# Kernel tuning notes

Hardware: AMD Instinct MI355X
Metric: run time of the kernel (lower is better)

The kernel has to match this reference:

```python
import jax, jax.numpy as jnp
import numpy as np

B, S, D = 2, 2048, 1024
H, DK = 16, 64
DFF = 4096
WINDOW = 128
GLOBAL = 16
EPS = 1e-5


def _layer_norm(x, g, b):
    mu = jnp.mean(x, axis=-1, keepdims=True)
    var = jnp.var(x, axis=-1, keepdims=True)
    return (x - mu) * jax.lax.rsqrt(var + EPS) * g + b


def setup_inputs() -> dict:
    key = jax.random.key(0)
    ks = jax.random.split(key, 12)
    s = 0.02
    inp = {
        "x": jax.random.normal(ks[0], (B, S, D), dtype=jnp.float32),
        "Wq": jax.random.normal(ks[1], (D, D), jnp.float32) * s,
        "bq": jnp.zeros((D,), jnp.float32),
        "Wk": jax.random.normal(ks[2], (D, D), jnp.float32) * s,
        "bk": jnp.zeros((D,), jnp.float32),
        "Wv": jax.random.normal(ks[3], (D, D), jnp.float32) * s,
        "bv": jnp.zeros((D,), jnp.float32),
        "Wo": jax.random.normal(ks[4], (D, D), jnp.float32) * s,
        "bo": jnp.zeros((D,), jnp.float32),
        "ln1_g": jnp.ones((D,), jnp.float32),
        "ln1_b": jnp.zeros((D,), jnp.float32),
        "W1": jax.random.normal(ks[5], (D, DFF), jnp.float32) * s,
        "b1": jnp.zeros((DFF,), jnp.float32),
        "W2": jax.random.normal(ks[6], (DFF, D), jnp.float32) * s,
        "b2": jnp.zeros((D,), jnp.float32),
        "ln2_g": jnp.ones((D,), jnp.float32),
        "ln2_b": jnp.zeros((D,), jnp.float32),
    }
    return inp


def _local_global_mask(seq_len):
    # token i attends to j iff |i-j| <= WINDOW, or i < GLOBAL, or j < GLOBAL
    i = jnp.arange(seq_len)[:, None]
    j = jnp.arange(seq_len)[None, :]
    m = jnp.abs(i - j) <= WINDOW
    m = m | (i < GLOBAL) | (j < GLOBAL)
    return m  # [S, S] bool


def reference(x, Wq, bq, Wk, bk, Wv, bv, Wo, bo, ln1_g, ln1_b,
              W1, b1, W2, b2, ln2_g, ln2_b):
    # --- self-attention sublayer (pre-norm residual) ---
    xn = _layer_norm(x, ln1_g, ln1_b)
    q = (xn @ Wq + bq).reshape(B, S, H, DK).transpose(0, 2, 1, 3)  # [B,H,S,DK]
    k = (xn @ Wk + bk).reshape(B, S, H, DK).transpose(0, 2, 1, 3)
    v = (xn @ Wv + bv).reshape(B, S, H, DK).transpose(0, 2, 1, 3)

    scores = jnp.einsum('bhqd,bhkd->bhqk', q, k) / jnp.sqrt(jnp.float32(DK))
    mask = _local_global_mask(S)  # [S,S]
    scores = jnp.where(mask[None, None], scores, jnp.float32(-jnp.inf))
    attn = jax.nn.softmax(scores, axis=-1)
    out = jnp.einsum('bhqk,bhkd->bhqd', attn, v)
    out = out.transpose(0, 2, 1, 3).reshape(B, S, D)
    out = out @ Wo + bo
    x = x + out

    # --- feed-forward sublayer (pre-norm residual) ---
    xn2 = _layer_norm(x, ln2_g, ln2_b)
    h = jax.nn.gelu(xn2 @ W1 + b1, approximate=False)
    ff = h @ W2 + b2
    x = x + ff
    return x
```

## Files before the change

kernel.cpp:

```cpp
#include <hip/hip_runtime.h>
#include <stdint.h>


typedef unsigned short u16;
typedef unsigned int   u32;
typedef __attribute__((ext_vector_type(8))) short  short8;
typedef __attribute__((ext_vector_type(4))) float  f32x4;

#define S_LEN   2048
#define D_MODEL 1024
#define ROWS    4096

__device__ __forceinline__ float bf2f(u16 u) {
  union { u32 i; float f; } v; v.i = ((u32)u) << 16; return v.f;
}
__device__ __forceinline__ float bflo(u32 u) {
  union { u32 i; float f; } v; v.i = u << 16; return v.f;
}
__device__ __forceinline__ float bfhi(u32 u) {
  union { u32 i; float f; } v; v.i = u & 0xffff0000u; return v.f;
}
__device__ __forceinline__ u16 f2bf(float f) {
  union { float f; u32 i; } v; v.f = f;
  u32 r = v.i + 0x7fffu + ((v.i >> 16) & 1u);
  return (u16)(r >> 16);
}

__device__ __forceinline__ void gld_lds16(const u16* g, u16* l) {
  __attribute__((address_space(3))) u32* lp =
      reinterpret_cast<__attribute__((address_space(3))) u32*>(
          reinterpret_cast<uintptr_t>(l));
  const __attribute__((address_space(1))) u32* gp =
      reinterpret_cast<const __attribute__((address_space(1))) u32*>(
          reinterpret_cast<uintptr_t>(g));
  __builtin_amdgcn_global_load_lds(gp, lp, 16, 0, 0);
}


#define GBAR  asm volatile("s_barrier" ::: "memory")
#define LGKM(n) asm volatile("s_waitcnt lgkmcnt(" #n ")" ::: "memory")
#define VM(n)   asm volatile("s_waitcnt vmcnt(" #n ")" ::: "memory")

#define STAGE_A(buf, t, hm) do {                                              \
    gld_lds16(pA##hm + (size_t)(t) * 64,      &Ald[buf][0][(hm)*4096 + ldst]);\
    gld_lds16(pA##hm + (size_t)(t) * 64 + 32, &Ald[buf][1][(hm)*4096 + ldst]);\
  } while (0)

#define STAGE_B(buf, t, hm) do {                                              \
    gld_lds16(pB##hm + (size_t)(t) * 64,      &Bld[buf][0][(hm)*4096 + ldst]);\
    gld_lds16(pB##hm + (size_t)(t) * 64 + 32, &Bld[buf][1][(hm)*4096 + ldst]);\
  } while (0)

#define READ_B(buf) do {                                                      \
    _Pragma("unroll") for (int nj = 0; nj < 4; ++nj) {                        \
      bfv[nj][0] = *(const short8*)&Bld[buf][0][brow + nj * 512];             \
      bfv[nj][1] = *(const short8*)&Bld[buf][1][brow + nj * 512]; }           \
  } while (0)

#define READ_A(buf, q) do {                                                   \
    af[(q)&1][0][0] = *(const short8*)&Ald[buf][0][arow + (2*(q)) * 512];     \
    af[(q)&1][0][1] = *(const short8*)&Ald[buf][1][arow + (2*(q)) * 512];     \
    af[(q)&1][1][0] = *(const short8*)&Ald[buf][0][arow + (2*(q)+1) * 512];   \
    af[(q)&1][1][1] = *(const short8*)&Ald[buf][1][arow + (2*(q)+1) * 512];   \
  } while (0)

#define MFMA_Q(q) do {                                                        \
    __builtin_amdgcn_s_setprio(1);                                            \
    _Pragma("unroll") for (int dm = 0; dm < 2; ++dm)                          \
    _Pragma("unroll") for (int kk = 0; kk < 2; ++kk)                          \
    _Pragma("unroll") for (int nj = 0; nj < 4; ++nj)                          \
      acc[2*(q)+dm][nj] = __builtin_amdgcn_mfma_f32_16x16x32_bf16(            \
          af[(q)&1][dm][kk], bfv[nj][kk], acc[2*(q)+dm][nj], 0, 0, 0);        \
    __builtin_amdgcn_s_setprio(0);                                            \
  } while (0)

template <int EPI, int KC, int LDK>
__global__ __launch_bounds__(512) void gemm256(
    const u16* __restrict__ A, const u16* __restrict__ Bt,
    const float* __restrict__ bias, u16* __restrict__ C0,
    u16* __restrict__ C1, int N)
{
  __shared__ __attribute__((aligned(16))) u16 Ald[2][2][256 * 32];
  __shared__ __attribute__((aligned(16))) u16 Bld[2][2][256 * 32];

  const int tid  = threadIdx.x;
  const int w    = tid >> 6;
  const int lane = tid & 63;
  const int wm   = w >> 2;
  const int wn   = w & 3;
  const int lm   = lane & 15;
  const int kq   = lane >> 4;
  const int bm   = blockIdx.y * 256;
  const int bn   = blockIdx.x * 256;
  const int kz   = blockIdx.z;

  const u16* Ak = A  + (size_t)kz * KC;
  const u16* Bk = Bt + (size_t)kz * KC;
  u16* C = kz ? C1 : C0;

  const int rslot = ((kq + (lm >> 1)) & 3) * 8;
  const int arow  = (wm * 128 + lm) * 32 + rslot;
  const int brow  = (wn * 64  + lm) * 32 + rslot;

  const int gcoff = (((lane & 3) - (lane >> 3)) & 3) * 8;
  const int srow  = w * 16 + (lane >> 2);
  const int ldst  = w * 512;

  const u16* pA0 = Ak + (size_t)(bm + srow) * LDK + gcoff;
  const u16* pA1 = pA0 + (size_t)128 * LDK;
  const u16* pB0 = Bk + (size_t)(bn + srow) * LDK + gcoff;
  const u16* pB1 = pB0 + (size_t)128 * LDK;

  f32x4 acc[8][4];
#pragma unroll
  for (int i = 0; i < 8; ++i)
#pragma unroll
    for (int j = 0; j < 4; ++j) acc[i][j] = (f32x4){0.f, 0.f, 0.f, 0.f};

  short8 af[2][2][2];
  short8 bfv[4][2];

  constexpr int P = KC >> 7;

  STAGE_B(0, 0, 0); STAGE_B(0, 0, 1);
  STAGE_A(0, 0, 0); STAGE_A(0, 0, 1);
  STAGE_B(1, 1, 0); STAGE_B(1, 1, 1);
  VM(4);
  GBAR;
  READ_A(0, 0);

  for (int i = 0; i < P - 1; ++i) {
    const int t1 = 2 * i + 1, t2 = 2 * i + 2, t3 = 2 * i + 3;
    GBAR; STAGE_A(1, t1, 0); READ_B(0); READ_A(0, 1); LGKM(4); MFMA_Q(0);
    GBAR; STAGE_A(1, t1, 1); READ_A(0, 2);            LGKM(4); MFMA_Q(1);
    GBAR; STAGE_B(0, t2, 0); READ_A(0, 3);            LGKM(4); MFMA_Q(2);
    VM(2);
    GBAR; STAGE_B(0, t2, 1); READ_A(1, 0);            LGKM(4); MFMA_Q(3);
    GBAR; STAGE_A(0, t2, 0); READ_B(1); READ_A(1, 1); LGKM(4); MFMA_Q(0);
    GBAR; STAGE_A(0, t2, 1); READ_A(1, 2);            LGKM(4); MFMA_Q(1);
    GBAR; STAGE_B(1, t3, 0); READ_A(1, 3);            LGKM(4); MFMA_Q(2);
    VM(2);
    GBAR; STAGE_B(1, t3, 1); READ_A(0, 0);            LGKM(4); MFMA_Q(3);
  }
  {
    const int t1 = 2 * P - 1;
    GBAR; STAGE_A(1, t1, 0); READ_B(0); READ_A(0, 1); LGKM(4); MFMA_Q(0);
    GBAR; STAGE_A(1, t1, 1); READ_A(0, 2);            LGKM(4); MFMA_Q(1);
    GBAR;                    READ_A(0, 3);            LGKM(4); MFMA_Q(2);
    VM(0);
    GBAR;                    READ_A(1, 0);            LGKM(4); MFMA_Q(3);
    GBAR;                    READ_B(1); READ_A(1, 1); LGKM(4); MFMA_Q(0);
    GBAR;                    READ_A(1, 2);            LGKM(4); MFMA_Q(1);
    GBAR;                    READ_A(1, 3);            LGKM(4); MFMA_Q(2);
    LGKM(0); MFMA_Q(3);
  }

  const int r0 = kq * 4;
#pragma unroll
  for (int mi = 0; mi < 8; ++mi) {
#pragma unroll
    for (int r = 0; r < 4; ++r) {
      const int grow = bm + wm * 128 + mi * 16 + r0 + r;
#pragma unroll
      for (int nj = 0; nj < 4; ++nj) {
        const int gcol = bn + wn * 64 + nj * 16 + lm;
        float v = acc[mi][nj][r];
        if (EPI < 2) v += bias[gcol];
        if (EPI == 1) v = 0.5f * v * (1.0f + erff(v * 0.70710678118654752f));
        C[(size_t)grow * N + gcol] = f2bf(v);
      }
    }
  }
}

__global__ __launch_bounds__(256) void reduce2(
    const u16* __restrict__ P0, const u16* __restrict__ P1,
    const float* __restrict__ bias, const float* res, float* out)
{
  const size_t base = ((size_t)blockIdx.x * 256 + threadIdx.x) * 8;
  const int col = (int)(base & 1023);
  uint4 p0 = *(const uint4*)(P0 + base);
  uint4 p1 = *(const uint4*)(P1 + base);
  float4 b0 = *(const float4*)(bias + col);
  float4 b1 = *(const float4*)(bias + col + 4);
  float4 r0 = *(const float4*)(res + base);
  float4 r1 = *(const float4*)(res + base + 4);
  float4 o0, o1;
  o0.x = bflo(p0.x) + bflo(p1.x) + b0.x + r0.x;
  o0.y = bfhi(p0.x) + bfhi(p1.x) + b0.y + r0.y;
  o0.z = bflo(p0.y) + bflo(p1.y) + b0.z + r0.z;
  o0.w = bfhi(p0.y) + bfhi(p1.y) + b0.w + r0.w;
  o1.x = bflo(p0.z) + bflo(p1.z) + b1.x + r1.x;
  o1.y = bfhi(p0.z) + bfhi(p1.z) + b1.y + r1.y;
  o1.z = bflo(p0.w) + bflo(p1.w) + b1.z + r1.z;
  o1.w = bfhi(p0.w) + bfhi(p1.w) + b1.w + r1.w;
  *(float4*)(out + base) = o0;
  *(float4*)(out + base + 4) = o1;
}

__global__ __launch_bounds__(256) void ln_kernel(
    const float* __restrict__ x, const float* __restrict__ g,
    const float* __restrict__ b, u16* __restrict__ o)
{
  const int row = blockIdx.x;
  const int t = threadIdx.x;
  float4 v = *(const float4*)(x + (size_t)row * D_MODEL + t * 4);
  float s  = v.x + v.y + v.z + v.w;
  float ss = v.x * v.x + v.y * v.y + v.z * v.z + v.w * v.w;
#pragma unroll
  for (int off = 32; off > 0; off >>= 1) {
    s  += __shfl_down(s, off);
    ss += __shfl_down(ss, off);
  }
  __shared__ float sm[4], ssm[4], stat[2];
  if ((t & 63) == 0) { sm[t >> 6] = s; ssm[t >> 6] = ss; }
  __syncthreads();
  if (t == 0) {
    float S = sm[0] + sm[1] + sm[2] + sm[3];
    float SS = ssm[0] + ssm[1] + ssm[2] + ssm[3];
    float mu = S * (1.0f / 1024.0f);
    float var = SS * (1.0f / 1024.0f) - mu * mu;
    stat[0] = mu;
    stat[1] = rsqrtf(fmaxf(var, 0.0f) + 1e-5f);
  }
  __syncthreads();
  const float mu = stat[0], rstd = stat[1];
  float4 gg = *(const float4*)(g + t * 4);
  float4 bb = *(const float4*)(b + t * 4);
  u16 o0 = f2bf((v.x - mu) * rstd * gg.x + bb.x);
  u16 o1 = f2bf((v.y - mu) * rstd * gg.y + bb.y);
  u16 o2 = f2bf((v.z - mu) * rstd * gg.z + bb.z);
  u16 o3 = f2bf((v.w - mu) * rstd * gg.w + bb.w);
  uint2 w;
  w.x = (u32)o0 | ((u32)o1 << 16);
  w.y = (u32)o2 | ((u32)o3 << 16);
  *(uint2*)(o + (size_t)row * D_MODEL + t * 4) = w;
}

__global__ __launch_bounds__(256) void attn_band(
    const u16* __restrict__ qkv, u16* __restrict__ out)
{
  const int t    = threadIdx.x;
  const int w    = t >> 6;
  const int lane = t & 63;
  const int m    = lane & 15;
  const int quad = lane >> 4;
  const int bh   = blockIdx.y;
  const int b    = bh >> 4, h = bh & 15;
  const int i0   = blockIdx.x * 64;
  const size_t bb = (size_t)b * S_LEN;

  __shared__ __attribute__((aligned(16))) u16 Ks[32 * 72];
  __shared__ __attribute__((aligned(16))) u16 Vt[64 * 40];
  __shared__ __attribute__((aligned(16))) u16 Ps[4][16 * 40];

  const u16* qrow = qkv + (bb + i0 + 16 * w + m) * 3072 + h * 64;
  const short8 aq0 = *(const short8*)(qrow + quad * 8);
  const short8 aq1 = *(const short8*)(qrow + 32 + quad * 8);

  f32x4 Ov[4];
#pragma unroll
  for (int td = 0; td < 4; ++td) Ov[td] = (f32x4){0.f, 0.f, 0.f, 0.f};
  float mP[4] = {-1e30f, -1e30f, -1e30f, -1e30f};
  float lS[4] = {0.f, 0.f, 0.f, 0.f};

  const int iB = i0 + 16 * w + quad * 4;

  const int lo = max(32, i0 - 128);
  const int hi = min(S_LEN, i0 + 192);
  const int nChunks = 1 + (hi - lo) / 32;

  const int skr = t >> 3;
  const int skc = (t & 7) * 8;

  for (int c = 0; c < nChunks; ++c) {
    const int j0 = (c == 0) ? 0 : lo + (c - 1) * 32;
    __syncthreads();
    {
      const u16* src = qkv + (bb + j0 + skr) * 3072 + 1024 + h * 64 + skc;
      uint4 kk = *(const uint4*)src;
      uint4 vv = *(const uint4*)(src + 1024);
      *(uint4*)&Ks[skr * 72 + skc] = kk;
      const u16 vs[8] = {
        (u16)(vv.x & 0xffffu), (u16)(vv.x >> 16),
        (u16)(vv.y & 0xffffu), (u16)(vv.y >> 16),
        (u16)(vv.z & 0xffffu), (u16)(vv.z >> 16),
        (u16)(vv.w & 0xffffu), (u16)(vv.w >> 16)};
#pragma unroll
      for (int i = 0; i < 8; ++i) Vt[(skc + i) * 40 + skr] = vs[i];
    }
    __syncthreads();

    const short8 b00 = *(const short8*)&Ks[m * 72 + quad * 8];
    const short8 b01 = *(const short8*)&Ks[m * 72 + 32 + quad * 8];
    const short8 b10 = *(const short8*)&Ks[(16 + m) * 72 + quad * 8];
    const short8 b11 = *(const short8*)&Ks[(16 + m) * 72 + 32 + quad * 8];
    f32x4 s0 = (f32x4){0.f, 0.f, 0.f, 0.f};
    f32x4 s1 = (f32x4){0.f, 0.f, 0.f, 0.f};
    s0 = __builtin_amdgcn_mfma_f32_16x16x32_bf16(aq0, b00, s0, 0, 0, 0);
    s0 = __builtin_amdgcn_mfma_f32_16x16x32_bf16(aq1, b01, s0, 0, 0, 0);
    s1 = __builtin_amdgcn_mfma_f32_16x16x32_bf16(aq0, b10, s1, 0, 0, 0);
    s1 = __builtin_amdgcn_mfma_f32_16x16x32_bf16(aq1, b11, s1, 0, 0, 0);

    const int jA = j0 + m, jB = j0 + 16 + m;
#pragma unroll
    for (int r = 0; r < 4; ++r) {
      const int iG = iB + r;
      const int da = iG - jA, db = iG - jB;
      s0[r] = ((jA < 16) || (da >= -128 && da <= 128)) ? s0[r] * 0.125f : -1e30f;
      s1[r] = ((jB < 16) || (db >= -128 && db <= 128)) ? s1[r] * 0.125f : -1e30f;
    }

    float al[4];
#pragma unroll
    for (int r = 0; r < 4; ++r) {
      float mx = fmaxf(s0[r], s1[r]);
      mx = fmaxf(mx, __shfl_xor(mx, 1, 16));
      mx = fmaxf(mx, __shfl_xor(mx, 2, 16));
      mx = fmaxf(mx, __shfl_xor(mx, 4, 16));
      mx = fmaxf(mx, __shfl_xor(mx, 8, 16));
      const float mn = fmaxf(mP[r], mx);
      al[r] = __expf(mP[r] - mn);
      mP[r] = mn;
      const float p0 = __expf(s0[r] - mn);
      const float p1 = __expf(s1[r] - mn);
      float ps = p0 + p1;
      ps += __shfl_xor(ps, 1, 16);
      ps += __shfl_xor(ps, 2, 16);
      ps += __shfl_xor(ps, 4, 16);
      ps += __shfl_xor(ps, 8, 16);
      lS[r] = lS[r] * al[r] + ps;
      Ps[w][(quad * 4 + r) * 40 + m]      = f2bf(p0);
      Ps[w][(quad * 4 + r) * 40 + 16 + m] = f2bf(p1);
    }
#pragma unroll
    for (int td = 0; td < 4; ++td)
#pragma unroll
      for (int r = 0; r < 4; ++r) Ov[td][r] *= al[r];

    const short8 pa = *(const short8*)&Ps[w][m * 40 + quad * 8];
#pragma unroll
    for (int td = 0; td < 4; ++td) {
      const short8 bv = *(const short8*)&Vt[(td * 16 + m) * 40 + quad * 8];
      Ov[td] = __builtin_amdgcn_mfma_f32_16x16x32_bf16(pa, bv, Ov[td], 0, 0, 0);
    }
  }

  if (i0 + 16 * w >= 16) {
    float inv[4];
#pragma unroll
    for (int r = 0; r < 4; ++r) inv[r] = 1.0f / lS[r];
#pragma unroll
    for (int td = 0; td < 4; ++td)
#pragma unroll
      for (int r = 0; r < 4; ++r)
        out[(bb + iB + r) * 1024 + h * 64 + td * 16 + m] =
            f2bf(Ov[td][r] * inv[r]);
  }
}

__global__ __launch_bounds__(256) void attn_gpart(
    const u16* __restrict__ qkv, float* __restrict__ Obuf,
    float* __restrict__ mbuf, float* __restrict__ lbuf)
{
  const int t    = threadIdx.x;
  const int w    = t >> 6;
  const int lane = t & 63;
  const int m    = lane & 15;
  const int quad = lane >> 4;
  const int kb   = blockIdx.x;
  const int bh   = blockIdx.y;
  const int b    = bh >> 4, h = bh & 15;
  const size_t bb = (size_t)b * S_LEN;

  __shared__ __attribute__((aligned(16))) u16 Ks[4][32 * 72];
  __shared__ __attribute__((aligned(16))) u16 Vt[4][64 * 40];
  __shared__ __attribute__((aligned(16))) u16 Ps[4][16 * 40];

  const u16* qrow = qkv + (bb + m) * 3072 + h * 64;
  const short8 aq0 = *(const short8*)(qrow + quad * 8);
  const short8 aq1 = *(const short8*)(qrow + 32 + quad * 8);

  f32x4 Ov[4];
#pragma unroll
  for (int td = 0; td < 4; ++td) Ov[td] = (f32x4){0.f, 0.f, 0.f, 0.f};
  float mP[4] = {-1e30f, -1e30f, -1e30f, -1e30f};
  float lS[4] = {0.f, 0.f, 0.f, 0.f};

  const int srow = lane >> 1;
  const int sd   = (lane & 1) * 32;

  for (int c = 0; c < 2; ++c) {
    const int j0 = kb * 256 + w * 64 + c * 32;
    {
      const u16* src = qkv + (bb + j0 + srow) * 3072 + 1024 + h * 64 + sd;
      uint4 k0 = *(const uint4*)(src);
      uint4 k1 = *(const uint4*)(src + 8);
      uint4 k2 = *(const uint4*)(src + 16);
      uint4 k3 = *(const uint4*)(src + 24);
      *(uint4*)&Ks[w][srow * 72 + sd]      = k0;
      *(uint4*)&Ks[w][srow * 72 + sd + 8]  = k1;
      *(uint4*)&Ks[w][srow * 72 + sd + 16] = k2;
      *(uint4*)&Ks[w][srow * 72 + sd + 24] = k3;
#pragma unroll
      for (int q4 = 0; q4 < 4; ++q4) {
        uint4 vv = *(const uint4*)(src + 1024 + q4 * 8);
        const u16 vs[8] = {
          (u16)(vv.x & 0xffffu), (u16)(vv.x >> 16),
          (u16)(vv.y & 0xffffu), (u16)(vv.y >> 16),
          (u16)(vv.z & 0xffffu), (u16)(vv.z >> 16),
          (u16)(vv.w & 0xffffu), (u16)(vv.w >> 16)};
#pragma unroll
        for (int i = 0; i < 8; ++i)
          Vt[w][(sd + q4 * 8 + i) * 40 + srow] = vs[i];
      }
    }

    const short8 b00 = *(const short8*)&Ks[w][m * 72 + quad * 8];
    const short8 b01 = *(const short8*)&Ks[w][m * 72 + 32 + quad * 8];
    const short8 b10 = *(const short8*)&Ks[w][(16 + m) * 72 + quad * 8];
    const short8 b11 = *(const short8*)&Ks[w][(16 + m) * 72 + 32 + quad * 8];
    f32x4 s0 = (f32x4){0.f, 0.f, 0.f, 0.f};
    f32x4 s1 = (f32x4){0.f, 0.f, 0.f, 0.f};
    s0 = __builtin_amdgcn_mfma_f32_16x16x32_bf16(aq0, b00, s0, 0, 0, 0);
    s0 = __builtin_amdgcn_mfma_f32_16x16x32_bf16(aq1, b01, s0, 0, 0, 0);
    s1 = __builtin_amdgcn_mfma_f32_16x16x32_bf16(aq0, b10, s1, 0, 0, 0);
    s1 = __builtin_amdgcn_mfma_f32_16x16x32_bf16(aq1, b11, s1, 0, 0, 0);

    float al[4];
#pragma unroll
    for (int r = 0; r < 4; ++r) {
      const float v0 = s0[r] * 0.125f, v1 = s1[r] * 0.125f;
      float mx = fmaxf(v0, v1);
      mx = fmaxf(mx, __shfl_xor(mx, 1, 16));
      mx = fmaxf(mx, __shfl_xor(mx, 2, 16));
      mx = fmaxf(mx, __shfl_xor(mx, 4, 16));
      mx = fmaxf(mx, __shfl_xor(mx, 8, 16));
      const float mn = fmaxf(mP[r], mx);
      al[r] = __expf(mP[r] - mn);
      mP[r] = mn;
      const float p0 = __expf(v0 - mn);
      const float p1 = __expf(v1 - mn);
      float ps = p0 + p1;
      ps += __shfl_xor(ps, 1, 16);
      ps += __shfl_xor(ps, 2, 16);
      ps += __shfl_xor(ps, 4, 16);
      ps += __shfl_xor(ps, 8, 16);
      lS[r] = lS[r] * al[r] + ps;
      Ps[w][(quad * 4 + r) * 40 + m]      = f2bf(p0);
      Ps[w][(quad * 4 + r) * 40 + 16 + m] = f2bf(p1);
    }
#pragma unroll
    for (int td = 0; td < 4; ++td)
#pragma unroll
      for (int r = 0; r < 4; ++r) Ov[td][r] *= al[r];

    const short8 pa = *(const short8*)&Ps[w][m * 40 + quad * 8];
#pragma unroll
    for (int td = 0; td < 4; ++td) {
      const short8 bv = *(const short8*)&Vt[w][(td * 16 + m) * 40 + quad * 8];
      Ov[td] = __builtin_amdgcn_mfma_f32_16x16x32_bf16(pa, bv, Ov[td], 0, 0, 0);
    }
  }

  const int p = kb * 4 + w;
  const size_t ob = ((size_t)(bh * 32 + p)) * 16 * 64;
#pragma unroll
  for (int td = 0; td < 4; ++td)
#pragma unroll
    for (int r = 0; r < 4; ++r)
      Obuf[ob + (size_t)(quad * 4 + r) * 64 + td * 16 + m] = Ov[td][r];
  if (m == 0) {
    const int mb = (bh * 32 + p) * 16;
#pragma unroll
    for (int r = 0; r < 4; ++r) {
      mbuf[mb + quad * 4 + r] = mP[r];
      lbuf[mb + quad * 4 + r] = lS[r];
    }
  }
}

__global__ __launch_bounds__(256) void attn_gcombine(
    const float* __restrict__ Obuf, const float* __restrict__ mbuf,
    const float* __restrict__ lbuf, u16* __restrict__ out)
{
  const int bh = blockIdx.x;
  const int b  = bh >> 4, h = bh & 15;
  const int t  = threadIdx.x;
  const int q  = t >> 4;
  const int d0 = (t & 15) * 4;
  const int mb = bh * 32 * 16;

  float mv[32];
  float M = -1e30f;
#pragma unroll
  for (int p = 0; p < 32; ++p) {
    mv[p] = mbuf[mb + p * 16 + q];
    M = fmaxf(M, mv[p]);
  }
  float L = 0.f;
  float4 acc = {0.f, 0.f, 0.f, 0.f};
#pragma unroll
  for (int p = 0; p < 32; ++p) {
    const float wp = __expf(mv[p] - M);
    L += lbuf[mb + p * 16 + q] * wp;
    float4 o = *(const float4*)&Obuf[(((size_t)(bh * 32 + p)) * 16 + q) * 64 + d0];
    acc.x += wp * o.x; acc.y += wp * o.y;
    acc.z += wp * o.z; acc.w += wp * o.w;
  }
  const float inv = 1.0f / L;
  uint2 wv;
  wv.x = (u32)f2bf(acc.x * inv) | ((u32)f2bf(acc.y * inv) << 16);
  wv.y = (u32)f2bf(acc.z * inv) | ((u32)f2bf(acc.w * inv) << 16);
  *(uint2*)(out + ((size_t)b * S_LEN + q) * 1024 + h * 64 + d0) = wv;
}

__global__ __launch_bounds__(256) void prep_all(
    const float* __restrict__ Wq, const float* __restrict__ Wk,
    const float* __restrict__ Wv, const float* __restrict__ Wo,
    const float* __restrict__ W1, const float* __restrict__ W2,
    const float* __restrict__ bq, const float* __restrict__ bk,
    const float* __restrict__ bv,
    u16* __restrict__ WQKVT, u16* __restrict__ WOT,
    u16* __restrict__ W1T, u16* __restrict__ W2T,
    float* __restrict__ BQKV)
{
  const int gb = blockIdx.x;
  const int t = threadIdx.x;
  if (gb >= 3072) {
    const int i = (gb - 3072) * 256 + t;
    if (i < 1024) BQKV[i] = bq[i];
    else if (i < 2048) BQKV[i] = bk[i - 1024];
    else BQKV[i] = bv[i - 2048];
    return;
  }
  const float* in; u16* outp; int R, Cc, bx, by;
  if (gb < 1024) {
    const int seg = gb >> 8, local = gb & 255;
    bx = local & 15; by = local >> 4; R = 1024; Cc = 1024;
    in   = (seg == 0) ? Wq : (seg == 1) ? Wk : (seg == 2) ? Wv : Wo;
    outp = (seg < 3) ? WQKVT + (size_t)seg * 1024 * 1024 : WOT;
  } else if (gb < 2048) {
    const int local = gb - 1024;
    bx = local & 63; by = local >> 6; R = 1024; Cc = 4096;
    in = W1; outp = W1T;
  } else {
    const int local = gb - 2048;
    bx = local & 15; by = local >> 4; R = 4096; Cc = 1024;
    in = W2; outp = W2T;
  }

  __shared__ u16 tile[64][65];
  const int tr = by * 64, tc = bx * 64;
  const int lr = t >> 2, lc0 = (t & 3) * 16;
  const float* src = in + (size_t)(tr + lr) * Cc + tc + lc0;
  float4 a0 = *(const float4*)(src);
  float4 a1 = *(const float4*)(src + 4);
  float4 a2 = *(const float4*)(src + 8);
  float4 a3 = *(const float4*)(src + 12);
  const float vals[16] = {a0.x, a0.y, a0.z, a0.w, a1.x, a1.y, a1.z, a1.w,
                          a2.x, a2.y, a2.z, a2.w, a3.x, a3.y, a3.z, a3.w};
#pragma unroll
  for (int q = 0; q < 16; ++q) tile[lr][lc0 + q] = f2bf(vals[q]);
  __syncthreads();
  u16* dst = outp + (size_t)(tc + lr) * R + tr + lc0;
  u32 w[8];
#pragma unroll
  for (int q = 0; q < 8; ++q)
    w[q] = (u32)tile[lc0 + 2 * q][lr] | ((u32)tile[lc0 + 2 * q + 1][lr] << 16);
  uint4 s0; s0.x = w[0]; s0.y = w[1]; s0.z = w[2]; s0.w = w[3];
  uint4 s1; s1.x = w[4]; s1.y = w[5]; s1.z = w[6]; s1.w = w[7];
  *(uint4*)dst = s0;
  *(uint4*)(dst + 8) = s1;
}

static const size_t OFF_WQKVT = 0;
static const size_t OFF_WOT   = OFF_WQKVT + (size_t)3072 * 1024 * 2;
static const size_t OFF_W1T   = OFF_WOT   + (size_t)1024 * 1024 * 2;
static const size_t OFF_W2T   = OFF_W1T   + (size_t)4096 * 1024 * 2;
static const size_t OFF_BQKV  = OFF_W2T   + (size_t)1024 * 4096 * 2;
static const size_t OFF_XN    = OFF_BQKV  + 16384;
static const size_t OFF_QKV   = OFF_XN    + (size_t)4096 * 1024 * 2;
static const size_t OFF_AO    = OFF_QKV   + (size_t)4096 * 3072 * 2;
static const size_t OFF_H     = OFF_QKV;

extern "C" void kernel_launch(void* const* d_in, const int* in_sizes, int n_in,
                              void* d_out, int out_size, void* d_ws, size_t ws_size,
                              hipStream_t stream)
{
  const float* x   = (const float*)d_in[0];
  const float* Wq  = (const float*)d_in[1];
  const float* bq  = (const float*)d_in[2];
  const float* Wk  = (const float*)d_in[3];
  const float* bk  = (const float*)d_in[4];
  const float* Wv  = (const float*)d_in[5];
  const float* bv  = (const float*)d_in[6];
  const float* Wo  = (const float*)d_in[7];
  const float* bo  = (const float*)d_in[8];
  const float* g1  = (const float*)d_in[9];
  const float* be1 = (const float*)d_in[10];
  const float* W1  = (const float*)d_in[11];
  const float* b1  = (const float*)d_in[12];
  const float* W2  = (const float*)d_in[13];
  const float* b2  = (const float*)d_in[14];
  const float* g2  = (const float*)d_in[15];
  const float* be2 = (const float*)d_in[16];
  float* outf = (float*)d_out;
  char* ws = (char*)d_ws;

  u16*   WQKVT = (u16*)(ws + OFF_WQKVT);
  u16*   WOT   = (u16*)(ws + OFF_WOT);
  u16*   W1T   = (u16*)(ws + OFF_W1T);
  u16*   W2T   = (u16*)(ws + OFF_W2T);
  float* BQKV  = (float*)(ws + OFF_BQKV);
  u16*   XN    = (u16*)(ws + OFF_XN);
  u16*   QKV   = (u16*)(ws + OFF_QKV);
  u16*   AO    = (u16*)(ws + OFF_AO);
  u16*   Hbuf  = (u16*)(ws + OFF_H);
  float* X1    = outf;
  u16* PWo0 = (u16*)(ws + OFF_QKV);
  u16* PWo1 = PWo0 + (size_t)4096 * 1024;
  u16* PW20 = (u16*)(ws + OFF_W1T);
  u16* PW21 = (u16*)(ws + OFF_XN);
  float* GO = (float*)(ws + OFF_XN);
  float* GM = GO + (size_t)32 * 32 * 16 * 64;
  float* GL = GM + 32 * 32 * 16;

  const dim3 blk(256);
  const dim3 blk512(512);
  prep_all<<<dim3(3084), blk, 0, stream>>>(Wq, Wk, Wv, Wo, W1, W2, bq, bk, bv,
                                           WQKVT, WOT, W1T, W2T, BQKV);

  ln_kernel<<<dim3(ROWS), blk, 0, stream>>>(x, g1, be1, XN);
  gemm256<0, 1024, 1024><<<dim3(12, 16, 1), blk512, 0, stream>>>(
      XN, WQKVT, BQKV, QKV, QKV, 3072);
  attn_band<<<dim3(32, 32), blk, 0, stream>>>(QKV, AO);
  attn_gpart<<<dim3(8, 32), blk, 0, stream>>>(QKV, GO, GM, GL);
  attn_gcombine<<<dim3(32), blk, 0, stream>>>(GO, GM, GL, AO);
  gemm256<2, 512, 1024><<<dim3(4, 16, 2), blk512, 0, stream>>>(
      AO, WOT, nullptr, PWo0, PWo1, 1024);
  reduce2<<<dim3(2048), blk, 0, stream>>>(PWo0, PWo1, bo, x, X1);

  ln_kernel<<<dim3(ROWS), blk, 0, stream>>>(X1, g2, be2, XN);
  gemm256<1, 1024, 1024><<<dim3(16, 16, 1), blk512, 0, stream>>>(
      XN, W1T, b1, Hbuf, Hbuf, 4096);
  gemm256<2, 2048, 4096><<<dim3(4, 16, 2), blk512, 0, stream>>>(
      Hbuf, W2T, nullptr, PW20, PW21, 1024);
  reduce2<<<dim3(2048), blk, 0, stream>>>(PW20, PW21, b2, X1, outf);
}
```

Baseline: 358.6 us.

## Load GEMM B operand directly to registers, stage only A through LDS

```diff
diff --git a/kernel.cpp b/kernel.cpp
--- a/kernel.cpp
+++ b/kernel.cpp
@@ -36,52 +36,54 @@
   __builtin_amdgcn_global_load_lds(gp, lp, 16, 0, 0);
 }
 
-
 #define GBAR  asm volatile("s_barrier" ::: "memory")
-#define LGKM(n) asm volatile("s_waitcnt lgkmcnt(" #n ")" ::: "memory")
-#define VM(n)   asm volatile("s_waitcnt vmcnt(" #n ")" ::: "memory")
+#define VM(n) asm volatile("s_waitcnt vmcnt(" #n ")" ::: "memory")
 
 #define STAGE_A(buf, t, hm) do {                                              \
     gld_lds16(pA##hm + (size_t)(t) * 64,      &Ald[buf][0][(hm)*4096 + ldst]);\
     gld_lds16(pA##hm + (size_t)(t) * 64 + 32, &Ald[buf][1][(hm)*4096 + ldst]);\
   } while (0)
 
-#define STAGE_B(buf, t, hm) do {                                              \
-    gld_lds16(pB##hm + (size_t)(t) * 64,      &Bld[buf][0][(hm)*4096 + ldst]);\
-    gld_lds16(pB##hm + (size_t)(t) * 64 + 32, &Bld[buf][1][(hm)*4096 + ldst]);\
+#define LOADB(BN, t) do {                                                     \
+    _Pragma("unroll") for (int nj = 0; nj < 4; ++nj) {                        \
+      BN[nj][0] = *(const short8*)(pBn[nj] + (size_t)(t) * 64);               \
+      BN[nj][1] = *(const short8*)(pBn[nj] + (size_t)(t) * 64 + 32);          \
+    }                                                                         \
   } while (0)
 
-#define READ_B(buf) do {                                                      \
-    _Pragma("unroll") for (int nj = 0; nj < 4; ++nj) {                        \
-      bfv[nj][0] = *(const short8*)&Bld[buf][0][brow + nj * 512];             \
-      bfv[nj][1] = *(const short8*)&Bld[buf][1][brow + nj * 512]; }           \
-  } while (0)
-
-#define READ_A(buf, q) do {                                                   \
-    af[(q)&1][0][0] = *(const short8*)&Ald[buf][0][arow + (2*(q)) * 512];     \
-    af[(q)&1][0][1] = *(const short8*)&Ald[buf][1][arow + (2*(q)) * 512];     \
-    af[(q)&1][1][0] = *(const short8*)&Ald[buf][0][arow + (2*(q)+1) * 512];   \
-    af[(q)&1][1][1] = *(const short8*)&Ald[buf][1][arow + (2*(q)+1) * 512];   \
-  } while (0)
-
-#define MFMA_Q(q) do {                                                        \
+#define TILE_COMPUTE(rb, BC) do {                                             \
     __builtin_amdgcn_s_setprio(1);                                            \
-    _Pragma("unroll") for (int dm = 0; dm < 2; ++dm)                          \
-    _Pragma("unroll") for (int kk = 0; kk < 2; ++kk)                          \
-    _Pragma("unroll") for (int nj = 0; nj < 4; ++nj)                          \
-      acc[2*(q)+dm][nj] = __builtin_amdgcn_mfma_f32_16x16x32_bf16(            \
-          af[(q)&1][dm][kk], bfv[nj][kk], acc[2*(q)+dm][nj], 0, 0, 0);        \
+    _Pragma("unroll") for (int mi = 0; mi < 8; ++mi) {                        \
+      short8 a0 = *(const short8*)&Ald[rb][0][arow + mi * 512];               \
+      short8 a1 = *(const short8*)&Ald[rb][1][arow + mi * 512];               \
+      _Pragma("unroll") for (int nj = 0; nj < 4; ++nj)                        \
+        acc[mi][nj] = __builtin_amdgcn_mfma_f32_16x16x32_bf16(                \
+            a0, BC[nj][0], acc[mi][nj], 0, 0, 0);                             \
+      _Pragma("unroll") for (int nj = 0; nj < 4; ++nj)                        \
+        acc[mi][nj] = __builtin_amdgcn_mfma_f32_16x16x32_bf16(                \
+            a1, BC[nj][1], acc[mi][nj], 0, 0, 0);                             \
+    }                                                                         \
     __builtin_amdgcn_s_setprio(0);                                            \
   } while (0)
 
+#define GTILE(t, rb, wb, BC, BN, LAST) do {                                   \
+    GBAR;                                                                     \
+    if (!(LAST)) {                                                            \
+      STAGE_A(wb, (t) + 1, 0); STAGE_A(wb, (t) + 1, 1);                       \
+      LOADB(BN, (t) + 1);                                                     \
+      VM(12);                                                                 \
+    } else { VM(0); }                                                         \
+    GBAR;                                                                     \
+    TILE_COMPUTE(rb, BC);                                                     \
+  } while (0)
+
 template <int EPI, int KC, int LDK>
-__global__ __launch_bounds__(512) void gemm256(
+__global__ __launch_bounds__(512, 1) void gemm256(
     const u16* __restrict__ A, const u16* __restrict__ Bt,
     const float* __restrict__ bias, u16* __restrict__ C0,
     u16* __restrict__ C1, int N)
 {
   __shared__ __attribute__((aligned(16))) u16 Ald[2][2][256 * 32];
-  __shared__ __attribute__((aligned(16))) u16 Bld[2][2][256 * 32];
 
   const int tid  = threadIdx.x;
   const int w    = tid >> 6;
@@ -100,7 +102,6 @@
 
   const int rslot = ((kq + (lm >> 1)) & 3) * 8;
   const int arow  = (wm * 128 + lm) * 32 + rslot;
-  const int brow  = (wn * 64  + lm) * 32 + rslot;
 
   const int gcoff = (((lane & 3) - (lane >> 3)) & 3) * 8;
   const int srow  = w * 16 + (lane >> 2);
@@ -108,8 +109,11 @@
 
   const u16* pA0 = Ak + (size_t)(bm + srow) * LDK + gcoff;
   const u16* pA1 = pA0 + (size_t)128 * LDK;
-  const u16* pB0 = Bk + (size_t)(bn + srow) * LDK + gcoff;
-  const u16* pB1 = pB0 + (size_t)128 * LDK;
+
+  const u16* pBn[4];
+#pragma unroll
+  for (int nj = 0; nj < 4; ++nj)
+    pBn[nj] = Bk + (size_t)(bn + wn * 64 + nj * 16 + lm) * LDK + kq * 8;
 
   f32x4 acc[8][4];
 #pragma unroll
@@ -117,43 +121,19 @@
 #pragma unroll
     for (int j = 0; j < 4; ++j) acc[i][j] = (f32x4){0.f, 0.f, 0.f, 0.f};
 
-  short8 af[2][2][2];
-  short8 bfv[4][2];
-
-  constexpr int P = KC >> 7;
-
-  STAGE_B(0, 0, 0); STAGE_B(0, 0, 1);
+  short8 b0[4][2], b1[4][2];
+
+  constexpr int NT = KC >> 6;
+
   STAGE_A(0, 0, 0); STAGE_A(0, 0, 1);
-  STAGE_B(1, 1, 0); STAGE_B(1, 1, 1);
-  VM(4);
-  GBAR;
-  READ_A(0, 0);
-
-  for (int i = 0; i < P - 1; ++i) {
-    const int t1 = 2 * i + 1, t2 = 2 * i + 2, t3 = 2 * i + 3;
-    GBAR; STAGE_A(1, t1, 0); READ_B(0); READ_A(0, 1); LGKM(4); MFMA_Q(0);
-    GBAR; STAGE_A(1, t1, 1); READ_A(0, 2);            LGKM(4); MFMA_Q(1);
-    GBAR; STAGE_B(0, t2, 0); READ_A(0, 3);            LGKM(4); MFMA_Q(2);
-    VM(2);
-    GBAR; STAGE_B(0, t2, 1); READ_A(1, 0);            LGKM(4); MFMA_Q(3);
-    GBAR; STAGE_A(0, t2, 0); READ_B(1); READ_A(1, 1); LGKM(4); MFMA_Q(0);
-    GBAR; STAGE_A(0, t2, 1); READ_A(1, 2);            LGKM(4); MFMA_Q(1);
-    GBAR; STAGE_B(1, t3, 0); READ_A(1, 3);            LGKM(4); MFMA_Q(2);
-    VM(2);
-    GBAR; STAGE_B(1, t3, 1); READ_A(0, 0);            LGKM(4); MFMA_Q(3);
-  }
-  {
-    const int t1 = 2 * P - 1;
-    GBAR; STAGE_A(1, t1, 0); READ_B(0); READ_A(0, 1); LGKM(4); MFMA_Q(0);
-    GBAR; STAGE_A(1, t1, 1); READ_A(0, 2);            LGKM(4); MFMA_Q(1);
-    GBAR;                    READ_A(0, 3);            LGKM(4); MFMA_Q(2);
-    VM(0);
-    GBAR;                    READ_A(1, 0);            LGKM(4); MFMA_Q(3);
-    GBAR;                    READ_B(1); READ_A(1, 1); LGKM(4); MFMA_Q(0);
-    GBAR;                    READ_A(1, 2);            LGKM(4); MFMA_Q(1);
-    GBAR;                    READ_A(1, 3);            LGKM(4); MFMA_Q(2);
-    LGKM(0); MFMA_Q(3);
-  }
+  LOADB(b0, 0);
+
+  for (int tp = 0; tp < NT / 2 - 1; ++tp) {
+    GTILE(2 * tp,     0, 1, b0, b1, false);
+    GTILE(2 * tp + 1, 1, 0, b1, b0, false);
+  }
+  GTILE(NT - 2, 0, 1, b0, b1, false);
+  GTILE(NT - 1, 1, 0, b1, b0, true);
 
   const int r0 = kq * 4;
 #pragma unroll
```

Result: slower. 443.3 us (+23.6%).
